# Optimization experiments

Hardware: AMD Instinct MI355X
Metric: run time of the kernel (lower is better)

The kernel has to match this reference:

```python
import jax, jax.numpy as jnp
import numpy as np

B, T, E, H = 1, 4096, 768, 12
DH = E // H


def setup_inputs() -> dict:
    key = jax.random.key(0)
    ks = jax.random.split(key, 10)
    s = 0.02
    inp = {
        "queries": jax.random.normal(ks[0], (B, T, E), jnp.float32),
        "values": jax.random.normal(ks[1], (B, T, E), jnp.float32),
        # causal mask (1 = keep, 0 = masked), matches masked_fill(mask == 0, -1e9)
        "mask": jnp.tril(jnp.ones((T, T), jnp.int32))[None, None, :, :],
        "Wq": jax.random.normal(ks[2], (E, E), jnp.float32) * s,
        "bq": jnp.zeros((E,), jnp.float32),
        "Wk": jax.random.normal(ks[3], (E, E), jnp.float32) * s,
        "bk": jnp.zeros((E,), jnp.float32),
        "Wv": jax.random.normal(ks[4], (E, E), jnp.float32) * s,
        "bv": jnp.zeros((E,), jnp.float32),
        "Wo": jax.random.normal(ks[5], (E, E), jnp.float32) * s,
        "bo": jnp.zeros((E,), jnp.float32),
    }
    return inp


def _split_heads(x):
    # [B,T,E] -> [B,H,T,DH]
    return x.reshape(B, T, H, DH).transpose(0, 2, 1, 3)


def reference(queries, values, mask, Wq, bq, Wk, bk, Wv, bv, Wo, bo):
    # torch nn.Linear: y = x @ W.T + b
    q = _split_heads(queries @ Wq.T + bq)
    k = _split_heads(values @ Wk.T + bk)
    v = _split_heads(values @ Wv.T + bv)
    scale = 1.0 / np.sqrt(DH).astype(np.float32)
    logits = jnp.einsum("bhqd,bhkd->bhqk", q, k) * scale  # [B,H,T,T]
    logits = jnp.where(mask == 0, jnp.float32(-1e9), logits)
    probs = jax.nn.softmax(logits, axis=-1)
    ctx = jnp.einsum("bhqk,bhkd->bhqd", probs, v)  # [B,H,T,DH]
    ctx = ctx.transpose(0, 2, 1, 3).reshape(B, T, E)
    return ctx @ Wo.T + bo
```

## Files before the change

kernel.cpp:

```cpp
#include <hip/hip_runtime.h>
#include <hip/hip_bf16.h>


typedef __hip_bfloat16 bf16;
typedef __attribute__((ext_vector_type(8))) short short8;
typedef __attribute__((ext_vector_type(4))) short short4v;
typedef __attribute__((ext_vector_type(4))) float f32x4;

#define TSEQ 4096
#define NHEAD 12
#define DHEAD 64
#define EMB 768

#if defined(__HIP_DEVICE_COMPILE__)
#define MFMA16(a, b, c) __builtin_amdgcn_mfma_f32_16x16x16bf16_1k(a, b, c, 0, 0, 0)
#else
#define MFMA16(a, b, c) (c)
#endif

typedef const __attribute__((address_space(1))) unsigned int* gptr_t;
typedef __attribute__((address_space(3))) unsigned int* lptr_t;

__device__ __forceinline__ void load_lds16(const void* g, void* l) {
    __builtin_amdgcn_global_load_lds((gptr_t)g, (lptr_t)l, 16, 0, 0);
}

__device__ __forceinline__ float b2f(short s) {
    unsigned u = ((unsigned)(unsigned short)s) << 16;
    float f;
    __builtin_memcpy(&f, &u, 4);
    return f;
}

__device__ __forceinline__ short f2bs(float f) {
    bf16 h = __float2bfloat16(f);
    short s;
    __builtin_memcpy(&s, &h, 2);
    return s;
}

struct CvtJob { const float* src; bf16* dst; int n; };
struct CvtArgs { CvtJob j[6]; };

__global__ __launch_bounds__(256) void cvt_kernel(CvtArgs a) {
    const CvtJob jb = a.j[blockIdx.y];
    const int i = (blockIdx.x * 256 + threadIdx.x) * 8;
    if (i >= jb.n) return;
    const float4 x0 = *(const float4*)(jb.src + i);
    const float4 x1 = *(const float4*)(jb.src + i + 4);
    bf16 tmp[8];
    tmp[0] = __float2bfloat16(x0.x); tmp[1] = __float2bfloat16(x0.y);
    tmp[2] = __float2bfloat16(x0.z); tmp[3] = __float2bfloat16(x0.w);
    tmp[4] = __float2bfloat16(x1.x); tmp[5] = __float2bfloat16(x1.y);
    tmp[6] = __float2bfloat16(x1.z); tmp[7] = __float2bfloat16(x1.w);
    *(short8*)(jb.dst + i) = *(const short8*)tmp;
}

__device__ __forceinline__ void gemm128(
    const bf16* __restrict__ A, const bf16* __restrict__ W,
    const float* __restrict__ bias,
    bf16* __restrict__ outb, float* __restrict__ outf,
    const int mode, const float scale, const int m0, const int n0,
    bf16* sA, bf16* sB)
{
    const int tid  = threadIdx.x;
    const int lane = tid & 63;
    const int wave = tid >> 6;
    const int wr = wave >> 1, wc = wave & 1;
    const int lg = lane >> 4, lr = lane & 15;

    f32x4 acc[4][4];
#pragma unroll
    for (int m = 0; m < 4; ++m)
#pragma unroll
        for (int n = 0; n < 4; ++n)
            acc[m][n] = (f32x4){0.f, 0.f, 0.f, 0.f};

    for (int k0 = 0; k0 < EMB; k0 += 64) {
        if (k0) __syncthreads();
#pragma unroll
        for (int is = 0; is < 4; ++is) {
            const int chunk = is * 256 + tid;
            const int row = chunk >> 3;
            const int csw = (chunk & 7) ^ (row & 7);
            load_lds16(A + (size_t)(m0 + row) * EMB + k0 + csw * 8,
                       sA + is * 2048 + wave * 512);
            load_lds16(W + (size_t)(n0 + row) * EMB + k0 + csw * 8,
                       sB + is * 2048 + wave * 512);
        }
        __syncthreads();

        short8 af[4][2], bfv[4][2];
#pragma unroll
        for (int m = 0; m < 4; ++m)
#pragma unroll
            for (int kk = 0; kk < 2; ++kk) {
                const int row = wr * 64 + m * 16 + lr;
                const int cc = (kk * 4 + lg) ^ (row & 7);
                af[m][kk] = *(const short8*)(sA + row * 64 + cc * 8);
            }
#pragma unroll
        for (int n = 0; n < 4; ++n)
#pragma unroll
            for (int kk = 0; kk < 2; ++kk) {
                const int row = wc * 64 + n * 16 + lr;
                const int cc = (kk * 4 + lg) ^ (row & 7);
                bfv[n][kk] = *(const short8*)(sB + row * 64 + cc * 8);
            }
#pragma unroll
        for (int kk = 0; kk < 2; ++kk)
#pragma unroll
            for (int m = 0; m < 4; ++m)
#pragma unroll
                for (int n = 0; n < 4; ++n)
                    acc[m][n] = __builtin_amdgcn_mfma_f32_16x16x32_bf16(
                        af[m][kk], bfv[n][kk], acc[m][n], 0, 0, 0);
    }

#pragma unroll
    for (int n = 0; n < 4; ++n) {
        const int o = n0 + wc * 64 + n * 16 + lr;
        const float bv = bias[o];
#pragma unroll
        for (int m = 0; m < 4; ++m) {
            const int tbase = m0 + wr * 64 + m * 16 + lg * 4;
#pragma unroll
            for (int r = 0; r < 4; ++r) {
                const float v = (acc[m][n][r] + bv) * scale;
                const int t = tbase + r;
                if (mode == 0)
                    outb[(size_t)(o >> 6) * TSEQ * DHEAD + (size_t)t * DHEAD + (o & 63)] =
                        __float2bfloat16(v);
                else if (mode == 1)
                    outb[(size_t)(o >> 6) * DHEAD * TSEQ + (size_t)(o & 63) * TSEQ + t] =
                        __float2bfloat16(v);
                else
                    outf[(size_t)t * EMB + o] = v;
            }
        }
    }
}

struct QkvArgs {
    const bf16 *xq, *xv, *Wq, *Wk, *Wv;
    const float *bq, *bk, *bv;
    bf16 *qo, *ko, *vto;
};

__global__ __launch_bounds__(256) void qkv_gemm(QkvArgs a) {
    __shared__ __attribute__((aligned(16))) bf16 sA[128 * 64];
    __shared__ __attribute__((aligned(16))) bf16 sB[128 * 64];
    const int z = blockIdx.z;
    const bf16* A = (z == 0) ? a.xq : a.xv;
    const bf16* W = (z == 0) ? a.Wq : (z == 1 ? a.Wk : a.Wv);
    const float* b = (z == 0) ? a.bq : (z == 1 ? a.bk : a.bv);
    bf16* o = (z == 0) ? a.qo : (z == 1 ? a.ko : a.vto);
    const int mode = (z == 2) ? 1 : 0;
    const float scale = (z == 0) ? 0.18033688011112042f : 1.0f;
    gemm128(A, W, b, o, nullptr, mode, scale, blockIdx.x * 128, blockIdx.y * 128, sA, sB);
}

__global__ __launch_bounds__(256) void out_gemm(
    const bf16* __restrict__ ctx, const bf16* __restrict__ Wo,
    const float* __restrict__ bo, float* __restrict__ out)
{
    __shared__ __attribute__((aligned(16))) bf16 sA[128 * 64];
    __shared__ __attribute__((aligned(16))) bf16 sB[128 * 64];
    gemm128(ctx, Wo, bo, nullptr, out, 2, 1.0f, blockIdx.x * 128, blockIdx.y * 128, sA, sB);
}

struct AttnState {
    f32x4 O[4];
    float m, l;
};

__device__ __forceinline__ void stage_tile(
    const bf16* __restrict__ Kh, const bf16* __restrict__ Vh,
    bf16* sK, bf16* sV, const int kv0, const int tid)
{
    const int wave = tid >> 6;
#pragma unroll
    for (int is = 0; is < 2; ++is) {
        const int chunk = is * 256 + tid;
        const int row = chunk >> 3;
        const int csw = (chunk & 7) ^ (row & 7);
        load_lds16(Kh + (size_t)(kv0 + row) * DHEAD + csw * 8,
                   sK + is * 2048 + wave * 512);
        load_lds16(Vh + (size_t)row * TSEQ + kv0 + csw * 8,
                   sV + is * 2048 + wave * 512);
    }
}

__device__ __forceinline__ void attn_tile(
    const bf16* sK, const bf16* sV,
    const short8 (&qf)[2], AttnState& st,
    const int kv0, const int qw, const int lane)
{
    const int lg = lane >> 4, lr = lane & 15;
    if (kv0 > qw + 15) return;

    f32x4 s[4];
#pragma unroll
    for (int n = 0; n < 4; ++n) s[n] = (f32x4){0.f, 0.f, 0.f, 0.f};
    short8 kf[4][2];
#pragma unroll
    for (int n = 0; n < 4; ++n)
#pragma unroll
        for (int kk = 0; kk < 2; ++kk) {
            const int row = n * 16 + lr;
            const int cc = (kk * 4 + lg) ^ (row & 7);
            kf[n][kk] = *(const short8*)(sK + row * 64 + cc * 8);
        }
#pragma unroll
    for (int kk = 0; kk < 2; ++kk)
#pragma unroll
        for (int n = 0; n < 4; ++n)
            s[n] = __builtin_amdgcn_mfma_f32_16x16x32_bf16(
                kf[n][kk], qf[kk], s[n], 0, 0, 0);

    if (kv0 + 63 > qw) {
        const int qi = qw + lr;
#pragma unroll
        for (int n = 0; n < 4; ++n) {
            const int kb = kv0 + n * 16 + lg * 4;
#pragma unroll
            for (int r = 0; r < 4; ++r)
                if (kb + r > qi) s[n][r] = -3.0e38f;
        }
    }

    float mx = s[0][0];
#pragma unroll
    for (int n = 0; n < 4; ++n)
#pragma unroll
        for (int r = 0; r < 4; ++r) mx = fmaxf(mx, s[n][r]);
    mx = fmaxf(mx, __shfl_xor(mx, 16));
    mx = fmaxf(mx, __shfl_xor(mx, 32));

    const float mn = fmaxf(st.m, mx);
    const float al = __builtin_amdgcn_exp2f(st.m - mn);
    st.m = mn;

    float rs = 0.f;
    short4v pq[4];
#pragma unroll
    for (int n = 0; n < 4; ++n) {
#pragma unroll
        for (int r = 0; r < 4; ++r) {
            const float p = __builtin_amdgcn_exp2f(s[n][r] - mn);
            s[n][r] = p;
            rs += p;
        }
        pq[n][0] = f2bs(s[n][0]); pq[n][1] = f2bs(s[n][1]);
        pq[n][2] = f2bs(s[n][2]); pq[n][3] = f2bs(s[n][3]);
    }
    rs += __shfl_xor(rs, 16);
    rs += __shfl_xor(rs, 32);
    st.l = st.l * al + rs;

#pragma unroll
    for (int nd = 0; nd < 4; ++nd)
#pragma unroll
        for (int r = 0; r < 4; ++r)
            st.O[nd][r] *= al;

#pragma unroll
    for (int nd = 0; nd < 4; ++nd) {
        const int row = nd * 16 + lr;
        f32x4 o = st.O[nd];
#pragma unroll
        for (int n = 0; n < 4; ++n) {
            const int c16 = (n * 2 + (lg >> 1)) ^ (row & 7);
            const short4v va = *(const short4v*)(sV + row * 64 + c16 * 8 + (lg & 1) * 4);
            o = MFMA16(va, pq[n], o);
        }
        st.O[nd] = o;
    }
}

__global__ __launch_bounds__(256, 4) void attn_kernel(
    const bf16* __restrict__ Q, const bf16* __restrict__ K,
    const bf16* __restrict__ VT, bf16* __restrict__ Opart,
    float* __restrict__ ml, const int nch)
{
    __shared__ __attribute__((aligned(16))) bf16 sK0[64 * 64];
    __shared__ __attribute__((aligned(16))) bf16 sK1[64 * 64];
    __shared__ __attribute__((aligned(16))) bf16 sV0[64 * 64];
    __shared__ __attribute__((aligned(16))) bf16 sV1[64 * 64];

    const int tid  = threadIdx.x;
    const int lane = tid & 63;
    const int wave = tid >> 6;
    const int lg = lane >> 4, lr = lane & 15;
    const int h  = blockIdx.z;
    const int c  = blockIdx.y;
    const int bx = gridDim.x - 1 - blockIdx.x;
    const int q0 = bx * 64;
    const int qw = q0 + wave * 16;

    const bf16* Qh = Q  + (size_t)h * TSEQ * DHEAD;
    const bf16* Kh = K  + (size_t)h * TSEQ * DHEAD;
    const bf16* Vh = VT + (size_t)h * DHEAD * TSEQ;

    const int S  = bx + 1;
    const int t0 = (c * S) / nch;
    const int t1 = ((c + 1) * S) / nch;

    short8 qf[2];
#pragma unroll
    for (int kk = 0; kk < 2; ++kk)
        qf[kk] = *(const short8*)(Qh + (size_t)(qw + lr) * DHEAD + kk * 32 + lg * 8);

    AttnState st;
#pragma unroll
    for (int nd = 0; nd < 4; ++nd) st.O[nd] = (f32x4){0.f, 0.f, 0.f, 0.f};
    st.m = -3.0e38f; st.l = 0.f;

    if (t0 < t1) stage_tile(Kh, Vh, sK0, sV0, t0 * 64, tid);
    __syncthreads();

    int it = t0;
    while (it < t1) {
        if (it + 1 < t1) stage_tile(Kh, Vh, sK1, sV1, (it + 1) * 64, tid);
        attn_tile(sK0, sV0, qf, st, it * 64, qw, lane);
        __syncthreads();
        ++it;
        if (it >= t1) break;
        if (it + 1 < t1) stage_tile(Kh, Vh, sK0, sV0, (it + 1) * 64, tid);
        attn_tile(sK1, sV1, qf, st, it * 64, qw, lane);
        __syncthreads();
        ++it;
    }

    const int u = (h * 64 + bx) * nch + c;
    bf16* op = Opart + (size_t)u * 4096;
    float* mlp = ml + (size_t)u * 128;
    const int q = wave * 16 + lr;
#pragma unroll
    for (int nd = 0; nd < 4; ++nd) {
        short4v ov;
        ov[0] = f2bs(st.O[nd][0]); ov[1] = f2bs(st.O[nd][1]);
        ov[2] = f2bs(st.O[nd][2]); ov[3] = f2bs(st.O[nd][3]);
        *(short4v*)(op + q * 64 + nd * 16 + lg * 4) = ov;
    }
    if (lg == 0) {
        mlp[q] = st.m;
        mlp[64 + q] = st.l;
    }
}

__global__ __launch_bounds__(256) void combine_kernel(
    const bf16* __restrict__ Opart, const float* __restrict__ ml,
    bf16* __restrict__ ctx, const int nch)
{
    const int h  = blockIdx.y;
    const int bx = blockIdx.x;
    const int tid = threadIdx.x;
    const int row = tid >> 2;
    const int dp  = (tid & 3) * 16;
    const int ub = (h * 64 + bx) * nch;

    float m[8], l[8], w[8];
    float M = -3.0e38f;
    for (int c = 0; c < nch; ++c) {
        m[c] = ml[(size_t)(ub + c) * 128 + row];
        l[c] = ml[(size_t)(ub + c) * 128 + 64 + row];
        M = fmaxf(M, m[c]);
    }
    float L = 0.f;
    for (int c = 0; c < nch; ++c) {
        w[c] = __builtin_amdgcn_exp2f(m[c] - M);
        L += l[c] * w[c];
    }
    const float invL = 1.0f / L;

    float acc[16];
#pragma unroll
    for (int i = 0; i < 16; ++i) acc[i] = 0.f;
    for (int c = 0; c < nch; ++c) {
        const bf16* op = Opart + ((size_t)(ub + c) * 64 + row) * 64 + dp;
        const short8 v0 = *(const short8*)op;
        const short8 v1 = *(const short8*)(op + 8);
#pragma unroll
        for (int i = 0; i < 8; ++i) acc[i] += w[c] * b2f(v0[i]);
#pragma unroll
        for (int i = 0; i < 8; ++i) acc[8 + i] += w[c] * b2f(v1[i]);
    }
    bf16 outv[16];
#pragma unroll
    for (int i = 0; i < 16; ++i) outv[i] = __float2bfloat16(acc[i] * invL);
    const int t = bx * 64 + row;
    bf16* dst = ctx + (size_t)t * EMB + h * DHEAD + dp;
    *(short8*)dst = *(const short8*)outv;
    *(short8*)(dst + 8) = *(const short8*)(outv + 8);
}

extern "C" void kernel_launch(void* const* d_in, const int* in_sizes, int n_in,
                              void* d_out, int out_size, void* d_ws, size_t ws_size,
                              hipStream_t stream) {
    const float* queries = (const float*)d_in[0];
    const float* values  = (const float*)d_in[1];
    const float* Wq = (const float*)d_in[3];
    const float* bq = (const float*)d_in[4];
    const float* Wk = (const float*)d_in[5];
    const float* bk = (const float*)d_in[6];
    const float* Wv = (const float*)d_in[7];
    const float* bv = (const float*)d_in[8];
    const float* Wo = (const float*)d_in[9];
    const float* bo = (const float*)d_in[10];
    float* out = (float*)d_out;

    const size_t NTE = (size_t)TSEQ * EMB;
    const size_t WSZ = (size_t)EMB * EMB;
    bf16* ws  = (bf16*)d_ws;
    bf16* qb  = ws;
    bf16* vb  = qb + NTE;
    bf16* wqb = vb + NTE;
    bf16* wkb = wqb + WSZ;
    bf16* wvb = wkb + WSZ;
    bf16* wob = wvb + WSZ;
    bf16* qh  = wob + WSZ;
    bf16* kh  = qh + NTE;
    bf16* vth = kh + NTE;
    bf16* ctx = qb;

    const size_t fixed_elems = 5 * NTE + 4 * WSZ;
    int nch = 8;
    for (;;) {
        const size_t units = (size_t)NHEAD * (TSEQ / 64) * nch;
        const size_t need = fixed_elems * 2 + units * 4096 * 2 + units * 128 * 4;
        if (ws_size >= need || nch == 1) break;
        nch = (nch == 8) ? 4 : 1;
    }
    const size_t units = (size_t)NHEAD * (TSEQ / 64) * nch;
    bf16* opart = ws + fixed_elems;
    float* ml = (float*)(opart + units * 4096);

    CvtArgs ca;
    ca.j[0] = {queries, qb,  (int)NTE};
    ca.j[1] = {values,  vb,  (int)NTE};
    ca.j[2] = {Wq,      wqb, (int)WSZ};
    ca.j[3] = {Wk,      wkb, (int)WSZ};
    ca.j[4] = {Wv,      wvb, (int)WSZ};
    ca.j[5] = {Wo,      wob, (int)WSZ};
    cvt_kernel<<<dim3((NTE + 2047) / 2048, 6), 256, 0, stream>>>(ca);

    QkvArgs a{qb, vb, wqb, wkb, wvb, bq, bk, bv, qh, kh, vth};
    qkv_gemm<<<dim3(TSEQ / 128, EMB / 128, 3), 256, 0, stream>>>(a);
    attn_kernel<<<dim3(TSEQ / 64, nch, NHEAD), 256, 0, stream>>>(qh, kh, vth, opart, ml, nch);
    combine_kernel<<<dim3(TSEQ / 64, NHEAD), 256, 0, stream>>>(opart, ml, ctx, nch);
    out_gemm<<<dim3(TSEQ / 128, EMB / 128), 256, 0, stream>>>(ctx, wob, bo, out);
}
```

Measured before the change: 138.7 us.

## Adapt split-KV chunk count per query block and narrow out-GEMM tiles

Attention blocks now choose their number of KV chunks from the causal length, at roughly one chunk per 8 tiles up to the maximum. Surplus chunk blocks exit early, so short rows no longer get split into tiny chunks that cost extra partial writes and combine traffic. The combine kernel reads only the chunks that were used and merges them in a single pass. The output projection GEMM is templated to 128x64 tiles, doubling its block count so more CUs are occupied on a 768-wide output, at the cost of reloading A tiles more often.

Result: faster. 127.2 us (-8.3%).

```diff
diff --git a/kernel.cpp b/kernel.cpp
--- a/kernel.cpp
+++ b/kernel.cpp
@@ -56,7 +56,8 @@
     *(short8*)(jb.dst + i) = *(const short8*)tmp;
 }
 
-__device__ __forceinline__ void gemm128(
+template<int NF>
+__device__ __forceinline__ void gemm_t(
     const bf16* __restrict__ A, const bf16* __restrict__ W,
     const float* __restrict__ bias,
     bf16* __restrict__ outb, float* __restrict__ outf,
@@ -69,11 +70,11 @@
     const int wr = wave >> 1, wc = wave & 1;
     const int lg = lane >> 4, lr = lane & 15;
 
-    f32x4 acc[4][4];
+    f32x4 acc[4][NF];
 #pragma unroll
     for (int m = 0; m < 4; ++m)
 #pragma unroll
-        for (int n = 0; n < 4; ++n)
+        for (int n = 0; n < NF; ++n)
             acc[m][n] = (f32x4){0.f, 0.f, 0.f, 0.f};
 
     for (int k0 = 0; k0 < EMB; k0 += 64) {
@@ -85,12 +86,18 @@
             const int csw = (chunk & 7) ^ (row & 7);
             load_lds16(A + (size_t)(m0 + row) * EMB + k0 + csw * 8,
                        sA + is * 2048 + wave * 512);
+        }
+#pragma unroll
+        for (int is = 0; is < NF; ++is) {
+            const int chunk = is * 256 + tid;
+            const int row = chunk >> 3;
+            const int csw = (chunk & 7) ^ (row & 7);
             load_lds16(W + (size_t)(n0 + row) * EMB + k0 + csw * 8,
                        sB + is * 2048 + wave * 512);
         }
         __syncthreads();
 
-        short8 af[4][2], bfv[4][2];
+        short8 af[4][2], bfv[NF][2];
 #pragma unroll
         for (int m = 0; m < 4; ++m)
 #pragma unroll
@@ -100,10 +107,10 @@
                 af[m][kk] = *(const short8*)(sA + row * 64 + cc * 8);
             }
 #pragma unroll
-        for (int n = 0; n < 4; ++n)
+        for (int n = 0; n < NF; ++n)
 #pragma unroll
             for (int kk = 0; kk < 2; ++kk) {
-                const int row = wc * 64 + n * 16 + lr;
+                const int row = wc * (NF * 16) + n * 16 + lr;
                 const int cc = (kk * 4 + lg) ^ (row & 7);
                 bfv[n][kk] = *(const short8*)(sB + row * 64 + cc * 8);
             }
@@ -112,14 +119,14 @@
 #pragma unroll
             for (int m = 0; m < 4; ++m)
 #pragma unroll
-                for (int n = 0; n < 4; ++n)
+                for (int n = 0; n < NF; ++n)
                     acc[m][n] = __builtin_amdgcn_mfma_f32_16x16x32_bf16(
                         af[m][kk], bfv[n][kk], acc[m][n], 0, 0, 0);
     }
 
 #pragma unroll
-    for (int n = 0; n < 4; ++n) {
-        const int o = n0 + wc * 64 + n * 16 + lr;
+    for (int n = 0; n < NF; ++n) {
+        const int o = n0 + wc * (NF * 16) + n * 16 + lr;
         const float bv = bias[o];
 #pragma unroll
         for (int m = 0; m < 4; ++m) {
@@ -157,7 +164,7 @@
     bf16* o = (z == 0) ? a.qo : (z == 1 ? a.ko : a.vto);
     const int mode = (z == 2) ? 1 : 0;
     const float scale = (z == 0) ? 0.18033688011112042f : 1.0f;
-    gemm128(A, W, b, o, nullptr, mode, scale, blockIdx.x * 128, blockIdx.y * 128, sA, sB);
+    gemm_t<4>(A, W, b, o, nullptr, mode, scale, blockIdx.x * 128, blockIdx.y * 128, sA, sB);
 }
 
 __global__ __launch_bounds__(256) void out_gemm(
@@ -165,8 +172,8 @@
     const float* __restrict__ bo, float* __restrict__ out)
 {
     __shared__ __attribute__((aligned(16))) bf16 sA[128 * 64];
-    __shared__ __attribute__((aligned(16))) bf16 sB[128 * 64];
-    gemm128(ctx, Wo, bo, nullptr, out, 2, 1.0f, blockIdx.x * 128, blockIdx.y * 128, sA, sB);
+    __shared__ __attribute__((aligned(16))) bf16 sB[64 * 64];
+    gemm_t<2>(ctx, Wo, bo, nullptr, out, 2, 1.0f, blockIdx.x * 128, blockIdx.y * 64, sA, sB);
 }
 
 struct AttnState {
@@ -281,7 +288,7 @@
 __global__ __launch_bounds__(256, 4) void attn_kernel(
     const bf16* __restrict__ Q, const bf16* __restrict__ K,
     const bf16* __restrict__ VT, bf16* __restrict__ Opart,
-    float* __restrict__ ml, const int nch)
+    float* __restrict__ ml, const int nch_max)
 {
     __shared__ __attribute__((aligned(16))) bf16 sK0[64 * 64];
     __shared__ __attribute__((aligned(16))) bf16 sK1[64 * 64];
@@ -298,14 +305,16 @@
     const int q0 = bx * 64;
     const int qw = q0 + wave * 16;
 
+    const int S = bx + 1;
+    const int nchb = (nch_max > 1) ? min((S + 7) >> 3, nch_max) : 1;
+    if (c >= nchb) return;
+    const int t0 = (c * S) / nchb;
+    const int t1 = ((c + 1) * S) / nchb;
+
     const bf16* Qh = Q  + (size_t)h * TSEQ * DHEAD;
     const bf16* Kh = K  + (size_t)h * TSEQ * DHEAD;
     const bf16* Vh = VT + (size_t)h * DHEAD * TSEQ;
 
-    const int S  = bx + 1;
-    const int t0 = (c * S) / nch;
-    const int t1 = ((c + 1) * S) / nch;
-
     short8 qf[2];
 #pragma unroll
     for (int kk = 0; kk < 2; ++kk)
@@ -316,7 +325,7 @@
     for (int nd = 0; nd < 4; ++nd) st.O[nd] = (f32x4){0.f, 0.f, 0.f, 0.f};
     st.m = -3.0e38f; st.l = 0.f;
 
-    if (t0 < t1) stage_tile(Kh, Vh, sK0, sV0, t0 * 64, tid);
+    stage_tile(Kh, Vh, sK0, sV0, t0 * 64, tid);
     __syncthreads();
 
     int it = t0;
@@ -332,7 +341,7 @@
         ++it;
     }
 
-    const int u = (h * 64 + bx) * nch + c;
+    const int u = (h * 64 + bx) * nch_max + c;
     bf16* op = Opart + (size_t)u * 4096;
     float* mlp = ml + (size_t)u * 128;
     const int q = wave * 16 + lr;
@@ -351,41 +360,40 @@
 
 __global__ __launch_bounds__(256) void combine_kernel(
     const bf16* __restrict__ Opart, const float* __restrict__ ml,
-    bf16* __restrict__ ctx, const int nch)
+    bf16* __restrict__ ctx, const int nch_max)
 {
     const int h  = blockIdx.y;
     const int bx = blockIdx.x;
     const int tid = threadIdx.x;
     const int row = tid >> 2;
     const int dp  = (tid & 3) * 16;
-    const int ub = (h * 64 + bx) * nch;
-
-    float m[8], l[8], w[8];
+    const int ub = (h * 64 + bx) * nch_max;
+    const int S = bx + 1;
+    const int nchb = (nch_max > 1) ? min((S + 7) >> 3, nch_max) : 1;
+
     float M = -3.0e38f;
-    for (int c = 0; c < nch; ++c) {
-        m[c] = ml[(size_t)(ub + c) * 128 + row];
-        l[c] = ml[(size_t)(ub + c) * 128 + 64 + row];
-        M = fmaxf(M, m[c]);
-    }
+    for (int c = 0; c < nchb; ++c)
+        M = fmaxf(M, ml[(size_t)(ub + c) * 128 + row]);
+
     float L = 0.f;
-    for (int c = 0; c < nch; ++c) {
-        w[c] = __builtin_amdgcn_exp2f(m[c] - M);
-        L += l[c] * w[c];
-    }
-    const float invL = 1.0f / L;
-
     float acc[16];
 #pragma unroll
     for (int i = 0; i < 16; ++i) acc[i] = 0.f;
-    for (int c = 0; c < nch; ++c) {
+    for (int c = 0; c < nchb; ++c) {
+        const float mc = ml[(size_t)(ub + c) * 128 + row];
+        const float lc = ml[(size_t)(ub + c) * 128 + 64 + row];
+        const float w = __builtin_amdgcn_exp2f(mc - M);
+        L += lc * w;
         const bf16* op = Opart + ((size_t)(ub + c) * 64 + row) * 64 + dp;
         const short8 v0 = *(const short8*)op;
         const short8 v1 = *(const short8*)(op + 8);
 #pragma unroll
-        for (int i = 0; i < 8; ++i) acc[i] += w[c] * b2f(v0[i]);
-#pragma unroll
-        for (int i = 0; i < 8; ++i) acc[8 + i] += w[c] * b2f(v1[i]);
-    }
+        for (int i = 0; i < 8; ++i) acc[i] += w * b2f(v0[i]);
+#pragma unroll
+        for (int i = 0; i < 8; ++i) acc[8 + i] += w * b2f(v1[i]);
+    }
+    const float invL = 1.0f / L;
+
     bf16 outv[16];
 #pragma unroll
     for (int i = 0; i < 16; ++i) outv[i] = __float2bfloat16(acc[i] * invL);
@@ -449,5 +457,5 @@
     qkv_gemm<<<dim3(TSEQ / 128, EMB / 128, 3), 256, 0, stream>>>(a);
     attn_kernel<<<dim3(TSEQ / 64, nch, NHEAD), 256, 0, stream>>>(qh, kh, vth, opart, ml, nch);
     combine_kernel<<<dim3(TSEQ / 64, NHEAD), 256, 0, stream>>>(opart, ml, ctx, nch);
-    out_gemm<<<dim3(TSEQ / 128, EMB / 128), 256, 0, stream>>>(ctx, wob, bo, out);
-}
+    out_gemm<<<dim3(TSEQ / 128, EMB / 64), 256, 0, stream>>>(ctx, wob, bo, out);
+}
```
